# Performance work log

Measured on AMD Instinct MI355X. Metric: run time of the kernel, lower is better.

Reference implementation:

```python
import jax, jax.numpy as jnp
import numpy as np

B, T, D = 4, 8160, 1024
N, H = 8, 128            # heads, units_per_head (D == N*H)
W = 12                   # block_size
LEFT_CTX = 13            # atten_left_context
L = LEFT_CTX - 1         # left context frames beyond current position
R = 0                    # atten_right_context
C = W + L + R            # context_size = 24
CAP = 50.0               # attention_logits_soft_capping


def _timing_signal(pos, channels):
    # sinusoidal embedding, channels even (1024)
    pos = pos.astype(jnp.float32)
    nt = channels // 2
    inc = np.log(10000.0) / max(nt - 1, 1)
    inv = jnp.exp(jnp.arange(nt, dtype=jnp.float32) * -inc)
    st = pos[:, :, None] * inv[None, None, :]
    return jnp.concatenate([jnp.sin(st), jnp.cos(st)], axis=2)


def _extract_block_context(x, block_size, left, right, pad_val):
    # x: [B, T, ...] -> [B, num_blocks, context_size, ...]
    pads = [(0, 0)] * x.ndim
    pads[1] = (left, right + block_size - 1)
    xp = jnp.pad(x, pads, constant_values=jnp.asarray(pad_val, x.dtype))
    frame_len = block_size + left + right
    num_frames = (xp.shape[1] - frame_len) // block_size + 1
    idx = jnp.arange(num_frames)[:, None] * block_size + jnp.arange(frame_len)[None, :]
    return jnp.take(xp, idx, axis=1)


def _convert_to_block(x, block_size):
    b, t = x.shape[0], x.shape[1]
    nb = t // block_size  # T chosen as multiple of block_size
    return x.reshape((b, nb, block_size) + x.shape[2:])


def setup_inputs() -> dict:
    key = jax.random.key(0)
    ks = jax.random.split(key, 6)
    x = jax.random.normal(ks[0], (B, T, D), dtype=jnp.float32)
    mask = jnp.ones((B, T), dtype=bool)
    i = jnp.arange(W)[:, None]
    j = jnp.arange(C)[None, :]
    causal_valid_mask = (j >= i) & (j - i <= L + R)  # [W, C]
    s = 1.0 / np.sqrt(D)
    wq = jax.random.normal(ks[1], (D, D), dtype=jnp.float32) * s
    wk = jax.random.normal(ks[2], (D, D), dtype=jnp.float32) * s
    wv = jax.random.normal(ks[3], (D, D), dtype=jnp.float32) * s
    pos_proj = jax.random.normal(ks[4], (D, N, H), dtype=jnp.float32) * s
    return {"x": x, "mask": mask, "causal_valid_mask": causal_valid_mask,
            "wq": wq, "wk": wk, "wv": wv, "pos_proj": pos_proj}


def reference(x, mask, causal_valid_mask, wq, wk, wv, pos_proj):
    b, t, d = x.shape
    u = t // W
    q = jnp.einsum('btd,df->btf', x, wq).reshape(b, t, N, H)
    k = jnp.einsum('btd,df->btf', x, wk).reshape(b, t, N, H)
    v = jnp.einsum('btd,df->btf', x, wv).reshape(b, t, N, H)

    q_blk = _convert_to_block(q, W) * (H ** -0.5)        # [B,U,W,N,H]
    k_ctx = _extract_block_context(k, W, L, R, 0.0)      # [B,U,C,N,H]
    v_ctx = _extract_block_context(v, W, L, R, 0.0)      # [B,U,C,N,H]

    # term A+C: content logits
    term_ac = jnp.einsum('BuwNH,BucNH->BNuwc', q_blk, k_ctx)

    # term B+D: relative position logits via skew trick
    pos = jnp.arange(L, -R - 1, -1)[None, :]             # [1, L+R+1]
    sin_emb = _timing_signal(pos, D)                     # [1, L+R+1, D]
    sin_emb = jnp.einsum('fd,dnh->fnh', sin_emb[0], pos_proj)  # [F,N,H]
    term_bd = jnp.einsum('BuwNH,FNH->BNuwF', q_blk, sin_emb)   # [B,N,U,W,F]
    term_bd = jnp.pad(term_bd, ((0, 0),) * 4 + ((0, C + 1 - (L + R + 1)),))
    term_bd = term_bd.reshape(b, N, u, W * (C + 1))[:, :, :, :W * C]
    term_bd = term_bd.reshape(b, N, u, W, C)

    logits = term_ac + term_bd
    logits = CAP * jnp.tanh(logits / CAP)

    mask_ctx = _extract_block_context(mask, W, L, R, False)    # [B,U,C]
    valid = mask_ctx[:, None, :, None, :] & causal_valid_mask[None, None, None, :, :]
    logits = jnp.where(valid, logits, jnp.asarray(-1e9, logits.dtype))
    probs = jax.nn.softmax(logits, axis=-1)              # [B,N,U,W,C]

    out = jnp.einsum('BNuwc,BucNH->BuwNH', probs, v_ctx)
    return out.reshape(b, u * W, N, H)[:, :t]            # [B,T,N,H]
```

## Files before the change

### kernel.cpp

```cpp
#include <hip/hip_runtime.h>
#include <cstdint>
#include <cstddef>


typedef __bf16 bf16_t;
typedef float  floatx4 __attribute__((ext_vector_type(4)));
typedef __bf16 bf16x8  __attribute__((ext_vector_type(8)));
typedef __bf16 bf16x4  __attribute__((ext_vector_type(4)));

#define GLDS16(gp, lp)                                                        \
  __builtin_amdgcn_global_load_lds(                                           \
      (const __attribute__((address_space(1))) void*)(gp),                    \
      (__attribute__((address_space(3))) void*)(lp), 16, 0, 0)

static constexpr int kT     = 8160;
static constexpr int kM     = 4 * kT;
static constexpr int kU     = kT / 12;
static constexpr int kNC    = 3200;

__global__ __launch_bounds__(256) void convert_x(const float* __restrict__ X,
                                                 bf16_t* __restrict__ Xb) {
  const size_t i = ((size_t)blockIdx.x * 256 + threadIdx.x) * 8;
  float4 a = *(const float4*)(X + i);
  float4 b = *(const float4*)(X + i + 4);
  bf16x8 o;
  o[0] = (bf16_t)a.x; o[1] = (bf16_t)a.y; o[2] = (bf16_t)a.z; o[3] = (bf16_t)a.w;
  o[4] = (bf16_t)b.x; o[5] = (bf16_t)b.y; o[6] = (bf16_t)b.z; o[7] = (bf16_t)b.w;
  *(bf16x8*)(Xb + i) = o;
}

__global__ __launch_bounds__(512) void posemb_k(const float* __restrict__ pp,
                                                float* __restrict__ pe) {
  __shared__ float st[1024];
  __shared__ float red[4][128];
  const int d   = blockIdx.x;
  const int fc  = blockIdx.y;
  const int tid = threadIdx.x;
  const float dpos = (float)d;
  for (int i = tid; i < 1024; i += 512) {
    int idx = i & 511;
    float freq = expf(-(float)idx * (9.2103403719761836f / 511.0f));
    float a = dpos * freq;
    st[i] = (i < 512) ? sinf(a) : cosf(a);
  }
  __syncthreads();
  const int part = tid >> 7;
  const int fl   = tid & 127;
  const int f    = fc * 128 + fl;
  float acc = 0.f;
  const int dd0 = part * 256;
  for (int dd = dd0; dd < dd0 + 256; ++dd)
    acc += st[dd] * pp[(size_t)dd * 1024 + f];
  red[part][fl] = acc;
  __syncthreads();
  if (tid < 128)
    pe[(size_t)d * 1024 + f] = red[0][fl] + red[1][fl] + red[2][fl] + red[3][fl];
}

__global__ __launch_bounds__(256) void transpose_w(const float* __restrict__ Wq,
                                                   const float* __restrict__ Wk,
                                                   const float* __restrict__ Wv,
                                                   bf16_t* __restrict__ Wt) {
  __shared__ float tile[64][65];
  const int g = blockIdx.z;
  const float* W = (g == 0) ? Wq : (g == 1) ? Wk : Wv;
  bf16_t* O = Wt + (size_t)g * 1024 * 1024;
  const int k0 = blockIdx.x * 64, n0 = blockIdx.y * 64;
  const int col = threadIdx.x & 63, r4 = threadIdx.x >> 6;
#pragma unroll
  for (int i = 0; i < 16; ++i) {
    int row = i * 4 + r4;
    tile[row][col] = W[(size_t)(k0 + row) * 1024 + n0 + col];
  }
  __syncthreads();
#pragma unroll
  for (int i = 0; i < 16; ++i) {
    int row = i * 4 + r4;
    O[(size_t)(n0 + row) * 1024 + k0 + col] = (bf16_t)tile[col][row];
  }
}

__global__ __launch_bounds__(256) void pe2w(const float* __restrict__ pe,
                                            bf16_t* __restrict__ Wt) {
  const int idx = blockIdx.x;
  const int tid = threadIdx.x;
  bf16_t* out = Wt + (size_t)(3072 + idx) * 1024;
  if (idx >= 104) {
    bf16x4 z = {};
    *(bf16x4*)(out + tid * 4) = z;
    return;
  }
  const int n = idx / 13, d = idx - n * 13;
  __shared__ float peh[128];
  if (tid < 128) peh[tid] = pe[(size_t)d * 1024 + n * 128 + tid];
  __syncthreads();
  float acc[4] = {};
  const bf16_t* wb = Wt + (size_t)(n * 128) * 1024 + tid * 4;
  for (int h = 0; h < 128; ++h) {
    bf16x4 w4 = *(const bf16x4*)(wb + (size_t)h * 1024);
    float s = peh[h];
    acc[0] += s * (float)w4[0];
    acc[1] += s * (float)w4[1];
    acc[2] += s * (float)w4[2];
    acc[3] += s * (float)w4[3];
  }
  bf16x4 o;
  o[0] = (bf16_t)acc[0]; o[1] = (bf16_t)acc[1];
  o[2] = (bf16_t)acc[2]; o[3] = (bf16_t)acc[3];
  *(bf16x4*)(out + tid * 4) = o;
}

__global__ __launch_bounds__(512, 2) void qkv_gemm(const bf16_t* __restrict__ X,
                                                   const bf16_t* __restrict__ Wt,
                                                   bf16_t* __restrict__ QKV) {
  __shared__ __align__(16) bf16_t lds[8][8192];

  const int flat = blockIdx.x;
  const int work = (flat & 7) * 208 + (flat >> 3);
  const int mt = work / 13, nt = work % 13;
  const int m0 = mt * 256, n0 = nt * 256;

  const int tid  = threadIdx.x;
  const int wave = tid >> 6;
  const int lane = tid & 63;
  const int wm   = wave >> 2;
  const int wn   = wave & 3;
  const int qd   = lane >> 4;
  const int lr   = lane & 15;

  const int rr  = tid >> 3;
  const int cg8 = ((tid & 7) ^ (rr & 7)) * 8;
  const bf16_t* aP[4];
  const bf16_t* bP[4];
  {
    int r2 = m0 + 128 + rr, r3 = m0 + 192 + rr;
    aP[0] = X + (size_t)(m0 + rr) * 1024 + cg8;
    aP[1] = X + (size_t)(m0 + 64 + rr) * 1024 + cg8;
    aP[2] = X + (size_t)(r2 < kM ? r2 : 0) * 1024 + cg8;
    aP[3] = X + (size_t)(r3 < kM ? r3 : 0) * 1024 + cg8;
    int s2 = n0 + 128 + rr, s3 = n0 + 192 + rr;
    bP[0] = Wt + (size_t)(n0 + rr) * 1024 + cg8;
    bP[1] = Wt + (size_t)(n0 + 64 + rr) * 1024 + cg8;
    bP[2] = Wt + (size_t)(s2 < kNC ? s2 : 0) * 1024 + cg8;
    bP[3] = Wt + (size_t)(s3 < kNC ? s3 : 0) * 1024 + cg8;
  }

#define STAGE_A(h, t)                                                          \
  do {                                                                         \
    bf16_t* d_ = &lds[((t) & 1) * 4 + (h)][wave * 512];                        \
    GLDS16(aP[2 * (h)]     + (size_t)(t) * 64, d_);                            \
    GLDS16(aP[2 * (h) + 1] + (size_t)(t) * 64, d_ + 4096);                     \
  } while (0)
#define STAGE_B(h, t)                                                          \
  do {                                                                         \
    bf16_t* d_ = &lds[((t) & 1) * 4 + 2 + (h)][wave * 512];                    \
    GLDS16(bP[2 * (h)]     + (size_t)(t) * 64, d_);                            \
    GLDS16(bP[2 * (h) + 1] + (size_t)(t) * 64, d_ + 4096);                     \
  } while (0)

  auto frag = [&](int slot, int r, int cb) -> bf16x8 {
    uint32_t off = (uint32_t)(r * 128 + cb) ^ (uint32_t)((r & 7) << 4);
    return *(const bf16x8*)((const char*)&lds[slot][0] + off);
  };

  floatx4 acc[8][4] = {};

  STAGE_A(0, 0); STAGE_A(1, 0); STAGE_B(0, 0); STAGE_B(1, 0);
  STAGE_B(0, 1); STAGE_B(1, 1);
  asm volatile("s_waitcnt vmcnt(4)" ::: "memory");
  __builtin_amdgcn_s_barrier();

  const int aslot0 = wm;
  const int bslot0 = 2 + (wn >> 1);
  const int brow0  = (wn & 1) * 64;

#pragma unroll 2
  for (int t = 0; t < 16; ++t) {
    const int par = (t & 1) * 4;
    bf16x8 bfrag[4][2];
#pragma unroll
    for (int p = 0; p < 4; ++p) {
      if (p == 0) {
#pragma unroll
        for (int in = 0; in < 4; ++in)
#pragma unroll
          for (int k2 = 0; k2 < 2; ++k2)
            bfrag[in][k2] =
                frag(par + bslot0, brow0 + in * 16 + lr, k2 * 64 + qd * 16);
      }
      bf16x8 afrag[2][2];
#pragma unroll
      for (int i = 0; i < 2; ++i)
#pragma unroll
        for (int k2 = 0; k2 < 2; ++k2)
          afrag[i][k2] =
              frag(par + aslot0, (2 * p + i) * 16 + lr, k2 * 64 + qd * 16);

      if (p == 0)      { if (t < 15) STAGE_A(0, t + 1); }
      else if (p == 1) { if (t < 15) STAGE_A(1, t + 1); }
      else if (p == 2) { if (t < 14) STAGE_B(0, t + 2); }
      else             { if (t < 14) STAGE_B(1, t + 2); }

      if (p == 3) {
        if (t < 14) asm volatile("s_waitcnt vmcnt(4)" ::: "memory");
        else        asm volatile("s_waitcnt vmcnt(0)" ::: "memory");
      }
      __builtin_amdgcn_s_barrier();
      asm volatile("s_waitcnt lgkmcnt(0)" ::: "memory");
      __builtin_amdgcn_sched_barrier(0);

      __builtin_amdgcn_s_setprio(1);
#pragma unroll
      for (int i = 0; i < 2; ++i)
#pragma unroll
        for (int in = 0; in < 4; ++in)
#pragma unroll
          for (int k2 = 0; k2 < 2; ++k2)
            acc[2 * p + i][in] = __builtin_amdgcn_mfma_f32_16x16x32_bf16(
                afrag[i][k2], bfrag[in][k2], acc[2 * p + i][in], 0, 0, 0);
      __builtin_amdgcn_s_setprio(0);
      __builtin_amdgcn_sched_barrier(0);
      __builtin_amdgcn_s_barrier();
    }
  }
#undef STAGE_A
#undef STAGE_B

  const int mBase = m0 + wm * 128 + qd * 4;
  const int nBase = n0 + wn * 64 + lr;
  if (m0 + 256 <= kM && n0 + 256 <= kNC) {
#pragma unroll
    for (int im = 0; im < 8; ++im)
#pragma unroll
      for (int in = 0; in < 4; ++in)
#pragma unroll
        for (int r = 0; r < 4; ++r)
          QKV[(size_t)(mBase + im * 16 + r) * kNC + nBase + in * 16] =
              (bf16_t)acc[im][in][r];
  } else {
#pragma unroll
    for (int im = 0; im < 8; ++im)
#pragma unroll
      for (int in = 0; in < 4; ++in)
#pragma unroll
        for (int r = 0; r < 4; ++r) {
          int m = mBase + im * 16 + r;
          int n = nBase + in * 16;
          if (m < kM && n < kNC)
            QKV[(size_t)m * kNC + n] = (bf16_t)acc[im][in][r];
        }
  }
}

__global__ __launch_bounds__(256) void attn_k(const bf16_t* __restrict__ QKV,
                                              float* __restrict__ OUT) {
  __shared__ bf16_t qs[12 * 136];
  __shared__ bf16_t ks[24 * 136];
  __shared__ float  vs[24 * 132];
  __shared__ float  qpes[156];
  __shared__ float  p[12 * 16];

  const int flat = blockIdx.x;
  const int xcd  = flat & 7;
  const int jj   = flat >> 3;
  const int u    = xcd * 85 + (jj % 85);
  const int rest = jj / 85;
  const int n    = rest & 7;
  const int b    = rest >> 3;
  const int tid  = threadIdx.x;
  const int t0   = u * 12 - 12;
  const size_t bbase = (size_t)b * kT;

  if (tid < 192) {
    int row = tid >> 4, ch = tid & 15;
    bf16x8 q8 = *(const bf16x8*)(QKV + (bbase + u * 12 + row) * kNC + n * 128 + ch * 8);
    *(bf16x8*)(qs + row * 136 + ch * 8) = q8;
  }
  for (int i = tid; i < 24 * 16; i += 256) {
    int row = i >> 4, ch = i & 15;
    int t = t0 + row;
    int ko = row * 136 + ch * 8;
    int vo = row * 132 + ch * 8;
    if (t < 0) {
      bf16x8 z = {};
      *(bf16x8*)(ks + ko) = z;
      float4 z4 = {};
      *(float4*)(vs + vo) = z4; *(float4*)(vs + vo + 4) = z4;
    } else {
      size_t base = (bbase + t) * kNC + n * 128 + ch * 8;
      bf16x8 k8 = *(const bf16x8*)(QKV + base + 1024);
      bf16x8 v8 = *(const bf16x8*)(QKV + base + 2048);
      *(bf16x8*)(ks + ko) = k8;
      float4 vl = { (float)v8[0], (float)v8[1], (float)v8[2], (float)v8[3] };
      float4 vh = { (float)v8[4], (float)v8[5], (float)v8[6], (float)v8[7] };
      *(float4*)(vs + vo) = vl; *(float4*)(vs + vo + 4) = vh;
    }
  }
  if (tid < 156) {
    int w = tid / 13, d = tid - w * 13;
    qpes[tid] = (float)QKV[(bbase + u * 12 + w) * kNC + 3072 + n * 13 + d];
  }
  __syncthreads();

  if (tid < 156) {
    int w = tid / 13, d = tid - w * 13;
    int t = u * 12 + w - d;
    float lg = -1e30f;
    if (t >= 0) {
      int cc = w - d + 12;
      const bf16_t* qp = qs + w * 136;
      const bf16_t* kp = ks + cc * 136;
      float acc = qpes[tid];
#pragma unroll
      for (int it = 0; it < 16; ++it) {
        bf16x8 q8 = *(const bf16x8*)(qp + it * 8);
        bf16x8 k8 = *(const bf16x8*)(kp + it * 8);
#pragma unroll
        for (int jx = 0; jx < 8; ++jx) acc += (float)q8[jx] * (float)k8[jx];
      }
      lg = 50.0f * tanhf(acc * 0.0017677669529663689f);
    }
    p[w * 16 + d] = lg;
  }
  __syncthreads();

  if (tid < 12) {
    float* pr = p + tid * 16;
    float mx = -1e30f;
#pragma unroll
    for (int d = 0; d < 13; ++d) mx = fmaxf(mx, pr[d]);
    float sum = 0.f;
    float e[13];
#pragma unroll
    for (int d = 0; d < 13; ++d) { e[d] = expf(pr[d] - mx); sum += e[d]; }
    float inv = 1.0f / sum;
#pragma unroll
    for (int d = 0; d < 13; ++d) pr[d] = e[d] * inv;
  }
  __syncthreads();

  for (int i = tid; i < 12 * 32; i += 256) {
    int w = i >> 5, c4 = i & 31;
    const float* pw = p + w * 16;
    float4 acc = {};
#pragma unroll
    for (int d = 0; d < 13; ++d) {
      float pd = pw[d];
      float4 v4 = *(const float4*)(vs + (w - d + 12) * 132 + c4 * 4);
      acc.x += pd * v4.x; acc.y += pd * v4.y;
      acc.z += pd * v4.z; acc.w += pd * v4.w;
    }
    *(float4*)(OUT + (bbase + u * 12 + w) * 1024 + n * 128 + c4 * 4) = acc;
  }
}

extern "C" void kernel_launch(void* const* d_in, const int* in_sizes, int n_in,
                              void* d_out, int out_size, void* d_ws, size_t ws_size,
                              hipStream_t stream) {
  const float* x  = (const float*)d_in[0];
  const float* wq = (const float*)d_in[3];
  const float* wk = (const float*)d_in[4];
  const float* wv = (const float*)d_in[5];
  const float* pp = (const float*)d_in[6];

  char* ws = (char*)d_ws;
  float*  pe  = (float*)ws;
  bf16_t* Wt  = (bf16_t*)(ws + (1u << 16));
  bf16_t* Xb  = (bf16_t*)(ws + (1u << 16) + 8u * 1024 * 1024);
  bf16_t* QKV = (bf16_t*)(ws + (1u << 16) + 8u * 1024 * 1024 +
                          (size_t)kM * 1024 * 2);
  float* out = (float*)d_out;

  convert_x<<<kM * 1024 / (256 * 8), 256, 0, stream>>>(x, Xb);
  posemb_k<<<dim3(13, 8), 512, 0, stream>>>(pp, pe);
  transpose_w<<<dim3(16, 16, 3), 256, 0, stream>>>(wq, wk, wv, Wt);
  pe2w<<<128, 256, 0, stream>>>(pe, Wt);
  qkv_gemm<<<1664, 512, 0, stream>>>(Xb, Wt, QKV);
  attn_k<<<21760, 256, 0, stream>>>(QKV, out);
}
```

Before: 586.3 us.

## Rewrite local attention to process 5-block strips with MFMA for QK and PV

The attention kernel now processes a strip of five blocks (60 queries, 80 context frames) per workgroup instead of one block. QK^T and P·V run on bf16 and f16 MFMA instructions over swizzled LDS tiles, and the softmax is done in registers with wave shuffles. V is transposed into LDS as fp16. The goal is to cut per-workgroup overhead, reuse overlapping K/V loads across blocks, and replace scalar FMA loops with matrix instructions. In exchange it computes masked-out logits and stores probabilities in fp16, which may affect accuracy.

After: 650.8 us. 1.11x slower.

```diff
diff --git a/kernel.cpp b/kernel.cpp
--- a/kernel.cpp
+++ b/kernel.cpp
@@ -7,6 +7,7 @@
 typedef float  floatx4 __attribute__((ext_vector_type(4)));
 typedef __bf16 bf16x8  __attribute__((ext_vector_type(8)));
 typedef __bf16 bf16x4  __attribute__((ext_vector_type(4)));
+typedef _Float16 f16x8 __attribute__((ext_vector_type(8)));
 
 #define GLDS16(gp, lp)                                                        \
   __builtin_amdgcn_global_load_lds(                                           \
@@ -254,103 +255,166 @@
 
 __global__ __launch_bounds__(256) void attn_k(const bf16_t* __restrict__ QKV,
                                               float* __restrict__ OUT) {
-  __shared__ bf16_t qs[12 * 136];
-  __shared__ bf16_t ks[24 * 136];
-  __shared__ float  vs[24 * 132];
-  __shared__ float  qpes[156];
-  __shared__ float  p[12 * 16];
-
-  const int flat = blockIdx.x;
-  const int xcd  = flat & 7;
-  const int jj   = flat >> 3;
-  const int u    = xcd * 85 + (jj % 85);
-  const int rest = jj / 85;
-  const int n    = rest & 7;
-  const int b    = rest >> 3;
+  __shared__ __align__(16) bf16_t  Ks[80 * 128];
+  __shared__ __align__(16) _Float16 Vt[128 * 128];
+  __shared__ __align__(16) unsigned char QP[64 * 256];
+  __shared__ float qpes[64 * 16];
+
+  bf16_t*   Qs = (bf16_t*)QP;
+  _Float16* Ps = (_Float16*)QP;
+
+  const int flat  = blockIdx.x;
+  const int work  = (flat & 7) * 544 + (flat >> 3);
+  const int strip = work >> 5;
+  const int rest  = work & 31;
+  const int n     = rest >> 2;
+  const int b     = rest & 3;
+  const int u0    = strip * 5;
+  const int t0    = u0 * 12 - 12;
+  const size_t bbase = (size_t)b * kT;
   const int tid  = threadIdx.x;
-  const int t0   = u * 12 - 12;
-  const size_t bbase = (size_t)b * kT;
-
-  if (tid < 192) {
-    int row = tid >> 4, ch = tid & 15;
-    bf16x8 q8 = *(const bf16x8*)(QKV + (bbase + u * 12 + row) * kNC + n * 128 + ch * 8);
-    *(bf16x8*)(qs + row * 136 + ch * 8) = q8;
-  }
-  for (int i = tid; i < 24 * 16; i += 256) {
+  const int mi   = tid >> 6;
+  const int lane = tid & 63;
+  const int qd   = lane >> 4;
+  const int lr   = lane & 15;
+
+  for (int i = tid; i < 64 * 16; i += 256) {
+    int row = i >> 4, ch = i & 15;
+    bf16x8 q8 = {};
+    if (row < 60)
+      q8 = *(const bf16x8*)(QKV + (bbase + (u0 * 12 + row)) * kNC + n * 128 + ch * 8);
+    int idx = (row * 128 + ch * 8) ^ ((row & 7) << 3);
+    *(bf16x8*)(Qs + idx) = q8;
+  }
+  for (int i = tid; i < 80 * 16; i += 256) {
     int row = i >> 4, ch = i & 15;
     int t = t0 + row;
-    int ko = row * 136 + ch * 8;
-    int vo = row * 132 + ch * 8;
-    if (t < 0) {
-      bf16x8 z = {};
-      *(bf16x8*)(ks + ko) = z;
-      float4 z4 = {};
-      *(float4*)(vs + vo) = z4; *(float4*)(vs + vo + 4) = z4;
-    } else {
-      size_t base = (bbase + t) * kNC + n * 128 + ch * 8;
-      bf16x8 k8 = *(const bf16x8*)(QKV + base + 1024);
-      bf16x8 v8 = *(const bf16x8*)(QKV + base + 2048);
-      *(bf16x8*)(ks + ko) = k8;
-      float4 vl = { (float)v8[0], (float)v8[1], (float)v8[2], (float)v8[3] };
-      float4 vh = { (float)v8[4], (float)v8[5], (float)v8[6], (float)v8[7] };
-      *(float4*)(vs + vo) = vl; *(float4*)(vs + vo + 4) = vh;
-    }
-  }
-  if (tid < 156) {
-    int w = tid / 13, d = tid - w * 13;
-    qpes[tid] = (float)QKV[(bbase + u * 12 + w) * kNC + 3072 + n * 13 + d];
-  }
-  __syncthreads();
-
-  if (tid < 156) {
-    int w = tid / 13, d = tid - w * 13;
-    int t = u * 12 + w - d;
-    float lg = -1e30f;
-    if (t >= 0) {
-      int cc = w - d + 12;
-      const bf16_t* qp = qs + w * 136;
-      const bf16_t* kp = ks + cc * 136;
-      float acc = qpes[tid];
-#pragma unroll
-      for (int it = 0; it < 16; ++it) {
-        bf16x8 q8 = *(const bf16x8*)(qp + it * 8);
-        bf16x8 k8 = *(const bf16x8*)(kp + it * 8);
-#pragma unroll
-        for (int jx = 0; jx < 8; ++jx) acc += (float)q8[jx] * (float)k8[jx];
+    bf16x8 k8 = {};
+    if (t >= 0 && t < kT)
+      k8 = *(const bf16x8*)(QKV + (bbase + t) * kNC + 1024 + n * 128 + ch * 8);
+    int idx = (row * 128 + ch * 8) ^ ((row & 7) << 3);
+    *(bf16x8*)(Ks + idx) = k8;
+  }
+  for (int i = tid; i < 96 * 16; i += 256) {
+    int c = i >> 4, ch = i & 15;
+    int t = t0 + c;
+    bf16x8 v8 = {};
+    if (c < 80 && t >= 0 && t < kT)
+      v8 = *(const bf16x8*)(QKV + (bbase + t) * kNC + 2048 + n * 128 + ch * 8);
+#pragma unroll
+    for (int jx = 0; jx < 8; ++jx) {
+      int h = ch * 8 + jx;
+      int idx = (h * 128 + c) ^ ((h & 7) << 3);
+      Vt[idx] = (_Float16)(float)v8[jx];
+    }
+  }
+  for (int i = tid; i < 780; i += 256) {
+    int m = i / 13, d = i - m * 13;
+    qpes[m * 16 + d] =
+        (float)QKV[(bbase + (u0 * 12 + m)) * kNC + 3072 + n * 13 + d];
+  }
+  __syncthreads();
+
+  floatx4 sAcc[2] = {};
+  {
+    bf16x8 aQ[4];
+    const int qrow = mi * 16 + lr;
+#pragma unroll
+    for (int kk = 0; kk < 4; ++kk) {
+      int idx = (qrow * 128 + kk * 32 + qd * 8) ^ ((qrow & 7) << 3);
+      aQ[kk] = *(const bf16x8*)(Qs + idx);
+    }
+#pragma unroll
+    for (int ci = 0; ci < 2; ++ci) {
+      int krow = (mi + ci) * 16 + lr;
+#pragma unroll
+      for (int kk = 0; kk < 4; ++kk) {
+        int idx = (krow * 128 + kk * 32 + qd * 8) ^ ((krow & 7) << 3);
+        bf16x8 bK = *(const bf16x8*)(Ks + idx);
+        sAcc[ci] = __builtin_amdgcn_mfma_f32_16x16x32_bf16(aQ[kk], bK, sAcc[ci], 0, 0, 0);
       }
-      lg = 50.0f * tanhf(acc * 0.0017677669529663689f);
-    }
-    p[w * 16 + d] = lg;
-  }
-  __syncthreads();
-
-  if (tid < 12) {
-    float* pr = p + tid * 16;
+    }
+  }
+
+  float pval[2][4];
+#pragma unroll
+  for (int r = 0; r < 4; ++r) {
+    const int m = mi * 16 + qd * 4 + r;
+    float sv[2]; bool val[2];
     float mx = -1e30f;
 #pragma unroll
-    for (int d = 0; d < 13; ++d) mx = fmaxf(mx, pr[d]);
-    float sum = 0.f;
-    float e[13];
-#pragma unroll
-    for (int d = 0; d < 13; ++d) { e[d] = expf(pr[d] - mx); sum += e[d]; }
-    float inv = 1.0f / sum;
-#pragma unroll
-    for (int d = 0; d < 13; ++d) pr[d] = e[d] * inv;
-  }
-  __syncthreads();
-
-  for (int i = tid; i < 12 * 32; i += 256) {
-    int w = i >> 5, c4 = i & 31;
-    const float* pw = p + w * 16;
-    float4 acc = {};
-#pragma unroll
-    for (int d = 0; d < 13; ++d) {
-      float pd = pw[d];
-      float4 v4 = *(const float4*)(vs + (w - d + 12) * 132 + c4 * 4);
-      acc.x += pd * v4.x; acc.y += pd * v4.y;
-      acc.z += pd * v4.z; acc.w += pd * v4.w;
-    }
-    *(float4*)(OUT + (bbase + u * 12 + w) * 1024 + n * 128 + c4 * 4) = acc;
+    for (int ci = 0; ci < 2; ++ci) {
+      int c = (mi + ci) * 16 + lr;
+      int d = m + 12 - c;
+      int t = t0 + c;
+      bool v = (d >= 0) && (d <= 12) && (t >= 0) && (m < 60);
+      int qidx = m * 16 + (v ? d : 0);
+      float s = (sAcc[ci][r] + qpes[qidx]) * 0.0017677669529663689f;
+      s = 50.0f * tanhf(s);
+      sv[ci] = v ? s : -1e30f;
+      val[ci] = v;
+      mx = fmaxf(mx, sv[ci]);
+    }
+    mx = fmaxf(mx, __shfl_xor(mx, 1));
+    mx = fmaxf(mx, __shfl_xor(mx, 2));
+    mx = fmaxf(mx, __shfl_xor(mx, 4));
+    mx = fmaxf(mx, __shfl_xor(mx, 8));
+    float e0 = val[0] ? __expf(sv[0] - mx) : 0.f;
+    float e1 = val[1] ? __expf(sv[1] - mx) : 0.f;
+    float sm = e0 + e1;
+    sm += __shfl_xor(sm, 1);
+    sm += __shfl_xor(sm, 2);
+    sm += __shfl_xor(sm, 4);
+    sm += __shfl_xor(sm, 8);
+    float inv = (sm > 0.f) ? 1.0f / sm : 0.f;
+    pval[0][r] = e0 * inv;
+    pval[1][r] = e1 * inv;
+  }
+
+  __syncthreads();
+  {
+    float4 z = {};
+    float4* p4 = (float4*)QP;
+    for (int i = tid; i < 1024; i += 256) p4[i] = z;
+  }
+  __syncthreads();
+#pragma unroll
+  for (int r = 0; r < 4; ++r) {
+    const int m = mi * 16 + qd * 4 + r;
+#pragma unroll
+    for (int ci = 0; ci < 2; ++ci) {
+      int c = (mi + ci) * 16 + lr;
+      int idx = (m * 128 + c) ^ ((m & 7) << 3);
+      Ps[idx] = (_Float16)pval[ci][r];
+    }
+  }
+  __syncthreads();
+
+  floatx4 oAcc[8] = {};
+  const int klo = mi >> 1;
+  const int khi = (16 * mi + 27) >> 5;
+  const int prow = mi * 16 + lr;
+  for (int kk = klo; kk <= khi; ++kk) {
+    int pidx = (prow * 128 + kk * 32 + qd * 8) ^ ((prow & 7) << 3);
+    f16x8 aP = *(const f16x8*)(Ps + pidx);
+#pragma unroll
+    for (int hf = 0; hf < 8; ++hf) {
+      int vrow = hf * 16 + lr;
+      int vidx = (vrow * 128 + kk * 32 + qd * 8) ^ ((vrow & 7) << 3);
+      f16x8 bV = *(const f16x8*)(Vt + vidx);
+      oAcc[hf] = __builtin_amdgcn_mfma_f32_16x16x32_f16(aP, bV, oAcc[hf], 0, 0, 0);
+    }
+  }
+
+#pragma unroll
+  for (int r = 0; r < 4; ++r) {
+    const int m = mi * 16 + qd * 4 + r;
+    if (m < 60) {
+      float* op = OUT + (bbase + (u0 * 12 + m)) * 1024 + n * 128 + lr;
+#pragma unroll
+      for (int hf = 0; hf < 8; ++hf)
+        op[hf * 16] = oAcc[hf][r];
+    }
   }
 }
 
@@ -376,5 +440,5 @@
   transpose_w<<<dim3(16, 16, 3), 256, 0, stream>>>(wq, wk, wv, Wt);
   pe2w<<<128, 256, 0, stream>>>(pe, Wt);
   qkv_gemm<<<1664, 512, 0, stream>>>(Xb, Wt, QKV);
-  attn_k<<<21760, 256, 0, stream>>>(QKV, out);
-}
+  attn_k<<<4352, 256, 0, stream>>>(QKV, out);
+}
```
